# Kernel optimization log

Measured on AMD Instinct MI355X. Metric: run time of the kernel, lower is better.

Reference implementation:

```python
import jax, jax.numpy as jnp
import numpy as np

# static sizes
B = 32          # graphs
NPER = 1024     # nodes per graph
N0 = B * NPER
F_IN = 128
H = 4           # heads
DH = 32         # per-head dim (128/4)
HID = H * DH    # 128
E = 524288      # edges (avg degree 16)
K1, K2, K3 = 512, 256, 128  # ceil(0.5*nper) per stage
NC = 10


def gcn_agg(h, src, dst, w, n):
    """GCNConv propagation: sym-normalized aggregation with self-loops.
    h: [n,F] already projected; w: [E] edge weight (0 for filtered edges)."""
    deg = jax.ops.segment_sum(w, dst, num_segments=n) + 1.0  # +1 self-loop
    dinv = jax.lax.rsqrt(deg)
    coef = dinv[src] * dinv[dst] * w                          # [E]
    agg = jax.ops.segment_sum(h[src] * coef[:, None], dst, num_segments=n)
    return agg + h / deg[:, None]  # self-loop term: dinv[i]^2 = 1/deg[i]


def mh_gcn(x, W, b, src, dst, w, n):
    """MAGPoolGCNLayer: per-head GCNConv (32->32), relu, concat heads."""
    h = jnp.einsum('nhd,hde->nhe', x.reshape(n, H, DH), W).reshape(n, HID)
    return jax.nn.relu(gcn_agg(h, src, dst, w, n) + b.reshape(HID))


def att_pool(x, src, dst, w, A, psW, psb, n, k):
    """MultiHeadAtt: standard att, complex score, concat pooling, global weight."""
    sub = x.reshape(n, H, DH)
    att = jnp.einsum('nhd,hd->nh', sub, A)            # per-head Linear(32,1)
    cat = (att[:, :, None] * sub).reshape(n, HID)     # score*sub, concat
    score = (gcn_agg(cat @ psW, src, dst, w, n) + psb)[:, 0]  # GCNConv(HID,1)
    nper = n // B
    _, idx = jax.lax.top_k(score.reshape(B, nper), k)  # per-graph topk
    perm = (idx + jnp.arange(B)[:, None] * nper).reshape(-1)
    xn = x[perm] * jnp.tanh(score[perm])[:, None]      # global att weighting
    # filter_adj: remap kept nodes, mask edges touching dropped nodes
    nmap = jnp.full((n,), -1, jnp.int32).at[perm].set(jnp.arange(B * k, dtype=jnp.int32))
    ns, nd = nmap[src], nmap[dst]
    wn = w * ((ns >= 0) & (nd >= 0)).astype(w.dtype)
    return xn, jnp.maximum(ns, 0), jnp.maximum(nd, 0), wn


def readout(x):
    # graphs are contiguous with equal node counts -> reshape readout
    xr = x.reshape(B, -1, x.shape[-1])
    return jnp.concatenate([xr.max(1), xr.mean(1)], axis=1)  # [B, 2*HID]


def setup_inputs():
    key = jax.random.key(0)
    ks = jax.random.split(key, 26)
    gid = jnp.repeat(jnp.arange(B, dtype=jnp.int32), E // B)
    src = jax.random.randint(ks[0], (E,), 0, NPER, dtype=jnp.int32) + gid * NPER
    dst = jax.random.randint(ks[1], (E,), 0, NPER, dtype=jnp.int32) + gid * NPER
    x = jax.random.normal(ks[2], (N0, F_IN), jnp.float32)
    s = 0.1
    def rn(k, shp):
        return jax.random.normal(k, shp, jnp.float32) * s
    return {
        'x': x, 'src': src, 'dst': dst,
        'W1': rn(ks[3], (H, DH, DH)), 'b1': rn(ks[4], (H, DH)), 'A1': rn(ks[5], (H, DH)),
        'ps1W': rn(ks[6], (HID, 1)), 'ps1b': rn(ks[7], (1,)),
        'W2': rn(ks[8], (H, DH, DH)), 'b2': rn(ks[9], (H, DH)), 'A2': rn(ks[10], (H, DH)),
        'ps2W': rn(ks[11], (HID, 1)), 'ps2b': rn(ks[12], (1,)),
        'W3': rn(ks[13], (H, DH, DH)), 'b3': rn(ks[14], (H, DH)), 'A3': rn(ks[15], (H, DH)),
        'ps3W': rn(ks[16], (HID, 1)), 'ps3b': rn(ks[17], (1,)),
        'l1W': rn(ks[18], (2 * HID, HID)), 'l1b': rn(ks[19], (HID,)),
        'l2W': rn(ks[20], (HID, HID // 2)), 'l2b': rn(ks[21], (HID // 2,)),
        'l3W': rn(ks[22], (HID // 2, NC)), 'l3b': rn(ks[23], (NC,)),
    }


def reference(x, src, dst, W1, b1, A1, ps1W, ps1b, W2, b2, A2, ps2W, ps2b,
              W3, b3, A3, ps3W, ps3b, l1W, l1b, l2W, l2b, l3W, l3b):
    w = jnp.ones((E,), x.dtype)
    h = mh_gcn(x, W1, b1, src, dst, w, N0)
    h, s1, d1, w1 = att_pool(h, src, dst, w, A1, ps1W, ps1b, N0, K1)
    r1 = readout(h)
    n1 = B * K1
    h = mh_gcn(h, W2, b2, s1, d1, w1, n1)
    h, s2, d2, w2 = att_pool(h, s1, d1, w1, A2, ps2W, ps2b, n1, K2)
    r2 = readout(h)
    n2 = B * K2
    h = mh_gcn(h, W3, b3, s2, d2, w2, n2)
    h, _, _, _ = att_pool(h, s2, d2, w2, A3, ps3W, ps3b, n2, K3)
    r3 = readout(h)
    z = r1 + r2 + r3                      # [B, 2*HID]
    z = jax.nn.relu(z @ l1W + l1b)        # dropout skipped (eval mode)
    z = jax.nn.relu(z @ l2W + l2b)
    return jax.nn.log_softmax(z @ l3W + l3b, axis=-1)
```

## Files before the change

### kernel.cpp

```cpp
#include <hip/hip_runtime.h>
#include <math.h>

#define BGR 32
#define NPER0 1024
#define N0 (BGR * NPER0)
#define FDIM 128
#define EDG 524288
#define K1 512
#define K2 256
#define K3 128
#define EBLK (EDG / 256)
#define SXP 36
#define CAP 64

__device__ __forceinline__ unsigned enc_f(float v) {
    unsigned u = __float_as_uint(v);
    return (u & 0x80000000u) ? ~u : (u | 0x80000000u);
}
__device__ __forceinline__ float dec_f(unsigned u) {
    return (u & 0x80000000u) ? __uint_as_float(u ^ 0x80000000u) : __uint_as_float(~u);
}

__global__ void zero_all(int* __restrict__ cntA, unsigned* __restrict__ rmax,
                         float* __restrict__ rsum) {
    int i = blockIdx.x * 256 + threadIdx.x;
    if (i < N0) cntA[i] = 0;
    if (i < 3 * BGR * FDIM) { rmax[i] = 0u; rsum[i] = 0.0f; }
}

__device__ __forceinline__ void proj_compute(float* __restrict__ hp, int nb, int t,
                                             const float* __restrict__ sW,
                                             const float* __restrict__ sxT) {
    const int fg = t >> 3, ng = t & 7, h = fg >> 3;
    const float* ap = sxT + h * 32 * SXP + ng * 4;
    const float* bp = sW + h * 1024 + (fg & 7) * 4;
    float4 acc0 = {0.f, 0.f, 0.f, 0.f}, acc1 = acc0, acc2 = acc0, acc3 = acc0;
#pragma unroll
    for (int k = 0; k < 32; k++) {
        float4 a = *(const float4*)(ap + k * SXP);
        float4 b = *(const float4*)(bp + k * 32);
        acc0.x = fmaf(a.x, b.x, acc0.x); acc0.y = fmaf(a.x, b.y, acc0.y);
        acc0.z = fmaf(a.x, b.z, acc0.z); acc0.w = fmaf(a.x, b.w, acc0.w);
        acc1.x = fmaf(a.y, b.x, acc1.x); acc1.y = fmaf(a.y, b.y, acc1.y);
        acc1.z = fmaf(a.y, b.z, acc1.z); acc1.w = fmaf(a.y, b.w, acc1.w);
        acc2.x = fmaf(a.z, b.x, acc2.x); acc2.y = fmaf(a.z, b.y, acc2.y);
        acc2.z = fmaf(a.z, b.z, acc2.z); acc2.w = fmaf(a.z, b.w, acc2.w);
        acc3.x = fmaf(a.w, b.x, acc3.x); acc3.y = fmaf(a.w, b.y, acc3.y);
        acc3.z = fmaf(a.w, b.z, acc3.z); acc3.w = fmaf(a.w, b.w, acc3.w);
    }
    float4* op = (float4*)(hp + (size_t)(nb + ng * 4) * FDIM + fg * 4);
    op[0] = acc0; op[32] = acc1; op[64] = acc2; op[96] = acc3;
}

__device__ __forceinline__ void pool_body(const float* __restrict__ ha,
                                          const int* __restrict__ perm,
                                          const float* __restrict__ mult, int k, int pb,
                                          unsigned* __restrict__ rmax,
                                          float* __restrict__ rsum,
                                          float* __restrict__ smax,
                                          float* __restrict__ ssum) {
    const int t = threadIdx.x;
    const int g = pb & 31;
    const int c = pb >> 5;
    const int f = t & 127, half = t >> 7;
    const int base = g * k + c * 8;
    float vmax = -1e30f, vsum = 0.0f;
#pragma unroll
    for (int j0 = 0; j0 < 4; j0++) {
        int newid = base + half + j0 * 2;
        int old = perm[newid];
        float m = mult[newid];
        float v = ha[(size_t)old * FDIM + f] * m;
        vmax = fmaxf(vmax, v);
        vsum += v;
    }
    if (half) { smax[f] = vmax; ssum[f] = vsum; }
    __syncthreads();
    if (!half) {
        vmax = fmaxf(vmax, smax[f]);
        vsum += ssum[f];
        atomicMax(&rmax[g * FDIM + f], enc_f(vmax));
        atomicAdd(&rsum[g * FDIM + f], vsum);
    }
}

__global__ void bin_proj1(const int* __restrict__ src, const int* __restrict__ dst,
                          int* __restrict__ cnt, int* __restrict__ slot,
                          const float* __restrict__ x, const float* __restrict__ W,
                          float* __restrict__ hp) {
    __shared__ __align__(16) float sW[4096];
    __shared__ __align__(16) float sxT[128 * SXP];
    const int t = threadIdx.x;
    if (blockIdx.x < EBLK) {
        int e = blockIdx.x * 256 + t;
        int s = src[e];
        int d = dst[e];
        int p = atomicAdd(&cnt[d], 1);
        if (p < CAP) slot[d * CAP + p] = s;
        return;
    }
    const int tb = blockIdx.x - EBLK;
    const int nb = (tb & 31) * NPER0 + (tb >> 5) * 32;
    for (int i = t; i < 4096; i += 256) sW[i] = W[i];
    for (int i = t; i < 4096; i += 256) {
        int node = i >> 7, dim = i & 127;
        sxT[dim * SXP + node] = x[(size_t)(nb + node) * FDIM + dim];
    }
    __syncthreads();
    proj_compute(hp, nb, t, sW, sxT);
}

__global__ void bin_proj_pool(const int* __restrict__ cnt_prev,
                              const int* __restrict__ slot_prev,
                              const int* __restrict__ nmap,
                              int* __restrict__ cnt_next, int* __restrict__ slot_next,
                              const float* __restrict__ ha, const int* __restrict__ perm,
                              const float* __restrict__ mult, const float* __restrict__ W,
                              float* __restrict__ hp, int ncomp, int ntiles, int kprev,
                              unsigned* __restrict__ rmax, float* __restrict__ rsum) {
    __shared__ __align__(16) float sW[4096];
    __shared__ __align__(16) float sxT[128 * SXP];
    const int t = threadIdx.x;
    if (blockIdx.x < ncomp) {
        const int w = t >> 6, lane = t & 63;
        const int b = (blockIdx.x & 31) * kprev + (blockIdx.x >> 5) * 4 + w;
        const int old = perm[b];
        const int c = min(cnt_prev[old], CAP);
        int a = -1;
        if (lane < c) a = nmap[slot_prev[(size_t)old * CAP + lane]];
        unsigned long long mk = __ballot(a >= 0);
        if (a >= 0) {
            int pos = __popcll(mk & ((1ull << lane) - 1ull));
            slot_next[(size_t)b * CAP + pos] = a;
        }
        if (lane == 0) cnt_next[b] = __popcll(mk);
        return;
    }
    if (blockIdx.x >= ncomp + ntiles) {
        pool_body(ha, perm, mult, kprev, blockIdx.x - (ncomp + ntiles), rmax, rsum,
                  sW, sW + 128);
        return;
    }
    const int tb = blockIdx.x - ncomp;
    const int nb = (tb & 31) * kprev + (tb >> 5) * 32;
    for (int i = t; i < 4096; i += 256) sW[i] = W[i];
    for (int i = t; i < 4096; i += 256) {
        int node = i >> 7, dim = i & 127;
        int newid = nb + node;
        sxT[dim * SXP + node] = ha[(size_t)perm[newid] * FDIM + dim] * mult[newid];
    }
    __syncthreads();
    proj_compute(hp, nb, t, sW, sxT);
}

__global__ void pool_kernel(const float* __restrict__ ha, const int* __restrict__ perm,
                            const float* __restrict__ mult, int k,
                            unsigned* __restrict__ rmax, float* __restrict__ rsum) {
    __shared__ float smax[128], ssum[128];
    pool_body(ha, perm, mult, k, blockIdx.x, rmax, rsum, smax, ssum);
}

__global__ void agg_kernel(const float* __restrict__ hp, const float* __restrict__ b,
                           const int* __restrict__ cnt, const int* __restrict__ slot,
                           const float* __restrict__ A, const float* __restrict__ psW,
                           float* __restrict__ ha, float* __restrict__ csd, int nper) {
    const int w = threadIdx.x >> 6;
    const int lane = threadIdx.x & 63;
    const int g = blockIdx.x & 31;
    const int chunk = blockIdx.x >> 5;
    const int i = g * nper + chunk * 4 + w;
    const int ci = cnt[i];
    const float di = rsqrtf((float)ci + 1.0f);
    const int c = min(ci, CAP);
    const float2* __restrict__ hp2 = (const float2*)hp;
    float2 self = hp2[(size_t)i * 64 + lane];
    float accx = self.x * di * di, accy = self.y * di * di;
    int idx = 0;
    float dv = 0.0f;
    if (lane < c) {
        idx = slot[i * CAP + lane];
        dv = rsqrtf((float)cnt[idx] + 1.0f);
    }
    int j = 0;
    for (; j + 3 < c; j += 4) {
        int s0 = __shfl(idx, j, 64);
        int s1 = __shfl(idx, j + 1, 64);
        int s2 = __shfl(idx, j + 2, 64);
        int s3 = __shfl(idx, j + 3, 64);
        float c0 = __shfl(dv, j, 64) * di;
        float c1 = __shfl(dv, j + 1, 64) * di;
        float c2 = __shfl(dv, j + 2, 64) * di;
        float c3 = __shfl(dv, j + 3, 64) * di;
        float2 v0 = hp2[(size_t)s0 * 64 + lane];
        float2 v1 = hp2[(size_t)s1 * 64 + lane];
        float2 v2 = hp2[(size_t)s2 * 64 + lane];
        float2 v3 = hp2[(size_t)s3 * 64 + lane];
        accx = fmaf(v0.x, c0, accx); accy = fmaf(v0.y, c0, accy);
        accx = fmaf(v1.x, c1, accx); accy = fmaf(v1.y, c1, accy);
        accx = fmaf(v2.x, c2, accx); accy = fmaf(v2.y, c2, accy);
        accx = fmaf(v3.x, c3, accx); accy = fmaf(v3.y, c3, accy);
    }
    for (; j < c; j++) {
        int s = __shfl(idx, j, 64);
        float co = __shfl(dv, j, 64) * di;
        float2 v = hp2[(size_t)s * 64 + lane];
        accx = fmaf(v.x, co, accx); accy = fmaf(v.y, co, accy);
    }
    float2 bb = ((const float2*)b)[lane];
    float2 o;
    o.x = fmaxf(accx + bb.x, 0.0f);
    o.y = fmaxf(accy + bb.y, 0.0f);
    ((float2*)ha)[(size_t)i * 64 + lane] = o;
    float2 Av = ((const float2*)A)[lane];
    float2 Pv = ((const float2*)psW)[lane];
    float a = o.x * Av.x + o.y * Av.y;
    float p = o.x * Pv.x + o.y * Pv.y;
#pragma unroll
    for (int d = 8; d > 0; d >>= 1) {
        a += __shfl_down(a, d, 16);
        p += __shfl_down(p, d, 16);
    }
    float part = a * p;
    part += __shfl_down(part, 16, 64);
    part += __shfl_down(part, 32, 64);
    if (lane == 0) csd[i] = part * di;
}

__global__ void score_kernel(const float* __restrict__ csd, const int* __restrict__ cnt,
                             const int* __restrict__ slot, const float* __restrict__ psb,
                             float* __restrict__ scout, int nper) {
    const int w = threadIdx.x >> 6;
    const int lane = threadIdx.x & 63;
    const int g = blockIdx.x & 31;
    const int chunk = blockIdx.x >> 5;
    const int i = g * nper + chunk * 4 + w;
    const int ci = cnt[i];
    const int c = min(ci, CAP);
    float v = 0.0f;
    if (lane < c) v = csd[slot[(size_t)i * CAP + lane]];
#pragma unroll
    for (int d = 32; d > 0; d >>= 1) v += __shfl_xor(v, d, 64);
    if (lane == 0)
        scout[i] = rsqrtf((float)ci + 1.0f) * (v + csd[i]) + psb[0];
}

__global__ void topk_kernel(const float* __restrict__ scin, int nper, int k,
                            int* __restrict__ nmap, int* __restrict__ perm,
                            float* __restrict__ mult) {
    __shared__ float sc[NPER0];
    __shared__ unsigned ukey[NPER0];
    __shared__ unsigned hist[256];
    __shared__ unsigned wtot[4];
    __shared__ unsigned sel[2];
    __shared__ int ctr[2];
    const int g = blockIdx.x, t = threadIdx.x;
    const int w = t >> 6, l = t & 63;
    const int gnb = g * nper;
    for (int i = t; i < nper; i += 256) {
        float v = scin[gnb + i];
        sc[i] = v;
        ukey[i] = enc_f(v);
    }
    if (t == 0) { sel[0] = 0u; sel[1] = (unsigned)k; }
    __syncthreads();
    for (int shift = 24; shift >= 0; shift -= 8) {
        hist[t] = 0u;
        __syncthreads();
        const unsigned prefix = sel[0];
        const unsigned need = sel[1];
        for (int i = t; i < nper; i += 256) {
            unsigned u = ukey[i];
            bool inp = (shift == 24) || ((u >> (shift + 8)) == (prefix >> (shift + 8)));
            int dig = inp ? (int)((u >> shift) & 255u) : -1;
            int cv = inp ? 1 : 0;
#pragma unroll
            for (int d = 1; d < 64; d <<= 1) {
                int od = __shfl_xor(dig, d, 64);
                int oc = __shfl_xor(cv, d, 64);
                if (od == dig) cv = ((l & d) == 0) ? (cv + oc) : 0;
            }
            if (dig >= 0 && cv > 0) atomicAdd(&hist[dig], (unsigned)cv);
        }
        __syncthreads();
        const unsigned h = hist[t];
        unsigned s = h;
#pragma unroll
        for (int off = 1; off < 64; off <<= 1) {
            unsigned v = __shfl_down(s, off, 64);
            if (l + off < 64) s += v;
        }
        if (l == 0) wtot[w] = s;
        __syncthreads();
        unsigned add = 0;
        for (int ww = w + 1; ww < 4; ww++) add += wtot[ww];
        const unsigned sfx = s + add;
        const unsigned gtr = sfx - h;
        if (sfx >= need && gtr < need) {
            sel[0] = prefix | ((unsigned)t << shift);
            sel[1] = need - gtr;
        }
        __syncthreads();
    }
    const unsigned T = sel[0];
    const int need = (int)sel[1];
    if (t == 0) { ctr[0] = 0; ctr[1] = k - need; }
    __syncthreads();
    for (int i = t; i < nper; i += 256) {
        unsigned u = ukey[i];
        int node = gnb + i;
        int newid = -1;
        if (u > T) {
            newid = g * k + atomicAdd(&ctr[0], 1);
        } else if (u == T) {
            int slot2 = atomicAdd(&ctr[1], 1);
            if (slot2 < k) newid = g * k + slot2;
        }
        nmap[node] = newid;
        if (newid >= 0) {
            perm[newid] = node;
            mult[newid] = tanhf(sc[i]);
        }
    }
}

__global__ void final_mlp(const unsigned* __restrict__ rmax, const float* __restrict__ rsum,
                          const float* __restrict__ l1W, const float* __restrict__ l1b,
                          const float* __restrict__ l2W, const float* __restrict__ l2b,
                          const float* __restrict__ l3W, const float* __restrict__ l3b,
                          float* __restrict__ out) {
    __shared__ float sz[256], s1[128], s2[64], s3[10], red[2];
    const int g = blockIdx.x, t = threadIdx.x;
    const int RS = BGR * FDIM;
    sz[t] = dec_f(rmax[g * FDIM + t]) + dec_f(rmax[RS + g * FDIM + t]) +
            dec_f(rmax[2 * RS + g * FDIM + t]);
    sz[t + 128] = rsum[g * FDIM + t] / (float)K1 + rsum[RS + g * FDIM + t] / (float)K2 +
                  rsum[2 * RS + g * FDIM + t] / (float)K3;
    __syncthreads();
    float acc = l1b[t];
    for (int i = 0; i < 256; i++) acc = fmaf(sz[i], l1W[i * 128 + t], acc);
    s1[t] = fmaxf(acc, 0.0f);
    __syncthreads();
    if (t < 64) {
        float a2 = l2b[t];
        for (int i = 0; i < 128; i++) a2 = fmaf(s1[i], l2W[i * 64 + t], a2);
        s2[t] = fmaxf(a2, 0.0f);
    }
    __syncthreads();
    if (t < 10) {
        float a3 = l3b[t];
        for (int i = 0; i < 64; i++) a3 = fmaf(s2[i], l3W[i * 10 + t], a3);
        s3[t] = a3;
    }
    __syncthreads();
    if (t == 0) {
        float m = -1e30f;
        for (int c = 0; c < 10; c++) m = fmaxf(m, s3[c]);
        float sum = 0.0f;
        for (int c = 0; c < 10; c++) sum += expf(s3[c] - m);
        red[0] = m;
        red[1] = logf(sum);
    }
    __syncthreads();
    if (t < 10) out[g * 10 + t] = s3[t] - red[0] - red[1];
}

extern "C" void kernel_launch(void* const* d_in, const int* in_sizes, int n_in,
                              void* d_out, int out_size, void* d_ws, size_t ws_size,
                              hipStream_t stream) {
    const float* x    = (const float*)d_in[0];
    const int* src0   = (const int*)d_in[1];
    const int* dst0   = (const int*)d_in[2];
    const float* W1   = (const float*)d_in[3];
    const float* b1   = (const float*)d_in[4];
    const float* A1   = (const float*)d_in[5];
    const float* ps1W = (const float*)d_in[6];
    const float* ps1b = (const float*)d_in[7];
    const float* W2   = (const float*)d_in[8];
    const float* b2   = (const float*)d_in[9];
    const float* A2   = (const float*)d_in[10];
    const float* ps2W = (const float*)d_in[11];
    const float* ps2b = (const float*)d_in[12];
    const float* W3   = (const float*)d_in[13];
    const float* b3   = (const float*)d_in[14];
    const float* A3   = (const float*)d_in[15];
    const float* ps3W = (const float*)d_in[16];
    const float* ps3b = (const float*)d_in[17];
    const float* l1W  = (const float*)d_in[18];
    const float* l1b  = (const float*)d_in[19];
    const float* l2W  = (const float*)d_in[20];
    const float* l2b  = (const float*)d_in[21];
    const float* l3W  = (const float*)d_in[22];
    const float* l3b  = (const float*)d_in[23];
    float* out = (float*)d_out;

    char* ws = (char*)d_ws;
    size_t o = 0;
    auto alloc = [&](size_t bytes) -> void* {
        void* p = ws + o;
        o += (bytes + 255) & ~(size_t)255;
        return p;
    };
    float*    hproj = (float*)alloc((size_t)N0 * FDIM * 4);
    float*    hact  = (float*)alloc((size_t)N0 * FDIM * 4);
    int*      cntA  = (int*)alloc(N0 * 4);
    int*      cntB  = (int*)alloc(BGR * K1 * 4);
    int*      cntC  = (int*)alloc(BGR * K2 * 4);
    int*      slotA = (int*)alloc((size_t)N0 * CAP * 4);
    int*      slotB = (int*)alloc((size_t)BGR * K1 * CAP * 4);
    int*      slotC = (int*)alloc((size_t)BGR * K2 * CAP * 4);
    float*    cs    = (float*)alloc(N0 * 4);
    float*    scb   = (float*)alloc(N0 * 4);
    int*      nmapA = (int*)alloc(N0 * 4);
    int*      nmapB = (int*)alloc(BGR * K1 * 4);
    int*      nmapC = (int*)alloc(BGR * K2 * 4);
    int*      perm  = (int*)alloc(BGR * K1 * 4);
    float*    mult  = (float*)alloc(BGR * K1 * 4);
    unsigned* rmax  = (unsigned*)alloc(3 * BGR * FDIM * 4);
    float*    rsum  = (float*)alloc(3 * BGR * FDIM * 4);

    const int n1 = BGR * K1, n2 = BGR * K2;
    const int RS = BGR * FDIM;

    zero_all<<<N0 / 256, 256, 0, stream>>>(cntA, rmax, rsum);
    bin_proj1<<<EBLK + N0 / 32, 256, 0, stream>>>(src0, dst0, cntA, slotA, x, W1, hproj);
    agg_kernel<<<N0 / 4, 256, 0, stream>>>(hproj, b1, cntA, slotA, A1, ps1W, hact, cs, NPER0);
    score_kernel<<<N0 / 4, 256, 0, stream>>>(cs, cntA, slotA, ps1b, scb, NPER0);
    topk_kernel<<<BGR, 256, 0, stream>>>(scb, NPER0, K1, nmapA, perm, mult);

    bin_proj_pool<<<n1 / 4 + n1 / 32 + BGR * K1 / 8, 256, 0, stream>>>(
        cntA, slotA, nmapA, cntB, slotB, hact, perm, mult, W2, hproj,
        n1 / 4, n1 / 32, K1, rmax, rsum);
    agg_kernel<<<n1 / 4, 256, 0, stream>>>(hproj, b2, cntB, slotB, A2, ps2W, hact, cs, K1);
    score_kernel<<<n1 / 4, 256, 0, stream>>>(cs, cntB, slotB, ps2b, scb, K1);
    topk_kernel<<<BGR, 256, 0, stream>>>(scb, K1, K2, nmapB, perm, mult);

    bin_proj_pool<<<n2 / 4 + n2 / 32 + BGR * K2 / 8, 256, 0, stream>>>(
        cntB, slotB, nmapB, cntC, slotC, hact, perm, mult, W3, hproj,
        n2 / 4, n2 / 32, K2, rmax + RS, rsum + RS);
    agg_kernel<<<n2 / 4, 256, 0, stream>>>(hproj, b3, cntC, slotC, A3, ps3W, hact, cs, K2);
    score_kernel<<<n2 / 4, 256, 0, stream>>>(cs, cntC, slotC, ps3b, scb, K2);
    topk_kernel<<<BGR, 256, 0, stream>>>(scb, K2, K3, nmapC, perm, mult);

    pool_kernel<<<BGR * K3 / 8, 256, 0, stream>>>(hact, perm, mult, K3,
                                                  rmax + 2 * RS, rsum + 2 * RS);
    final_mlp<<<BGR, 128, 0, stream>>>(rmax, rsum, l1W, l1b, l2W, l2b, l3W, l3b, out);

    (void)in_sizes; (void)n_in; (void)out_size; (void)ws_size;
}
```

Before: 253.3 us.

## Fuse final pool into MLP kernel, coarsen pool blocks, reorder edge binning

The last-stage readout pool is folded into final_mlp, which now runs 256 threads per graph and reduces the kept nodes directly. This drops one launch and the third rmax/rsum atomic buffer. Pool blocks in bin_proj_pool now cover 32 nodes instead of 8, so there are fewer blocks and fewer atomics. Edge binning blocks are interleaved across graphs, which may spread atomic contention on cnt. The cost is less parallelism in the fused final kernel, where each of 32 blocks reads 128 rows serially.

```diff
diff --git a/kernel.cpp b/kernel.cpp
--- a/kernel.cpp
+++ b/kernel.cpp
@@ -10,6 +10,7 @@
 #define K2 256
 #define K3 128
 #define EBLK (EDG / 256)
+#define EPG (EDG / BGR)
 #define SXP 36
 #define CAP 64
 
@@ -25,7 +26,7 @@
                          float* __restrict__ rsum) {
     int i = blockIdx.x * 256 + threadIdx.x;
     if (i < N0) cntA[i] = 0;
-    if (i < 3 * BGR * FDIM) { rmax[i] = 0u; rsum[i] = 0.0f; }
+    if (i < 2 * BGR * FDIM) { rmax[i] = 0u; rsum[i] = 0.0f; }
 }
 
 __device__ __forceinline__ void proj_compute(float* __restrict__ hp, int nb, int t,
@@ -63,10 +64,10 @@
     const int g = pb & 31;
     const int c = pb >> 5;
     const int f = t & 127, half = t >> 7;
-    const int base = g * k + c * 8;
+    const int base = g * k + c * 32;
     float vmax = -1e30f, vsum = 0.0f;
 #pragma unroll
-    for (int j0 = 0; j0 < 4; j0++) {
+    for (int j0 = 0; j0 < 16; j0++) {
         int newid = base + half + j0 * 2;
         int old = perm[newid];
         float m = mult[newid];
@@ -92,7 +93,8 @@
     __shared__ __align__(16) float sxT[128 * SXP];
     const int t = threadIdx.x;
     if (blockIdx.x < EBLK) {
-        int e = blockIdx.x * 256 + t;
+        const int g = blockIdx.x & 31, chunk = blockIdx.x >> 5;
+        int e = g * EPG + chunk * 256 + t;
         int s = src[e];
         int d = dst[e];
         int p = atomicAdd(&cnt[d], 1);
@@ -153,13 +155,6 @@
     proj_compute(hp, nb, t, sW, sxT);
 }
 
-__global__ void pool_kernel(const float* __restrict__ ha, const int* __restrict__ perm,
-                            const float* __restrict__ mult, int k,
-                            unsigned* __restrict__ rmax, float* __restrict__ rsum) {
-    __shared__ float smax[128], ssum[128];
-    pool_body(ha, perm, mult, k, blockIdx.x, rmax, rsum, smax, ssum);
-}
-
 __global__ void agg_kernel(const float* __restrict__ hp, const float* __restrict__ b,
                            const int* __restrict__ cnt, const int* __restrict__ slot,
                            const float* __restrict__ A, const float* __restrict__ psW,
@@ -323,22 +318,42 @@
     }
 }
 
-__global__ void final_mlp(const unsigned* __restrict__ rmax, const float* __restrict__ rsum,
+__global__ void final_mlp(const float* __restrict__ ha, const int* __restrict__ perm,
+                          const float* __restrict__ mult,
+                          const unsigned* __restrict__ rmax, const float* __restrict__ rsum,
                           const float* __restrict__ l1W, const float* __restrict__ l1b,
                           const float* __restrict__ l2W, const float* __restrict__ l2b,
                           const float* __restrict__ l3W, const float* __restrict__ l3b,
                           float* __restrict__ out) {
-    __shared__ float sz[256], s1[128], s2[64], s3[10], red[2];
+    __shared__ float sz[256], s1[128], s2[64], s3[10], red[2], sm2[128], ss2[128];
     const int g = blockIdx.x, t = threadIdx.x;
     const int RS = BGR * FDIM;
-    sz[t] = dec_f(rmax[g * FDIM + t]) + dec_f(rmax[RS + g * FDIM + t]) +
-            dec_f(rmax[2 * RS + g * FDIM + t]);
-    sz[t + 128] = rsum[g * FDIM + t] / (float)K1 + rsum[RS + g * FDIM + t] / (float)K2 +
-                  rsum[2 * RS + g * FDIM + t] / (float)K3;
-    __syncthreads();
-    float acc = l1b[t];
-    for (int i = 0; i < 256; i++) acc = fmaf(sz[i], l1W[i * 128 + t], acc);
-    s1[t] = fmaxf(acc, 0.0f);
+    const int f = t & 127, half = t >> 7;
+    float vmax = -1e30f, vsum = 0.0f;
+#pragma unroll 8
+    for (int j0 = 0; j0 < 64; j0++) {
+        int newid = g * K3 + half + j0 * 2;
+        int old = perm[newid];
+        float m = mult[newid];
+        float v = ha[(size_t)old * FDIM + f] * m;
+        vmax = fmaxf(vmax, v);
+        vsum += v;
+    }
+    if (half) { sm2[f] = vmax; ss2[f] = vsum; }
+    __syncthreads();
+    if (!half) {
+        vmax = fmaxf(vmax, sm2[f]);
+        vsum += ss2[f];
+        sz[f] = dec_f(rmax[g * FDIM + f]) + dec_f(rmax[RS + g * FDIM + f]) + vmax;
+        sz[f + 128] = rsum[g * FDIM + f] / (float)K1 + rsum[RS + g * FDIM + f] / (float)K2 +
+                      vsum / (float)K3;
+    }
+    __syncthreads();
+    if (t < 128) {
+        float acc = l1b[t];
+        for (int i = 0; i < 256; i++) acc = fmaf(sz[i], l1W[i * 128 + t], acc);
+        s1[t] = fmaxf(acc, 0.0f);
+    }
     __syncthreads();
     if (t < 64) {
         float a2 = l2b[t];
@@ -415,8 +430,8 @@
     int*      nmapC = (int*)alloc(BGR * K2 * 4);
     int*      perm  = (int*)alloc(BGR * K1 * 4);
     float*    mult  = (float*)alloc(BGR * K1 * 4);
-    unsigned* rmax  = (unsigned*)alloc(3 * BGR * FDIM * 4);
-    float*    rsum  = (float*)alloc(3 * BGR * FDIM * 4);
+    unsigned* rmax  = (unsigned*)alloc(2 * BGR * FDIM * 4);
+    float*    rsum  = (float*)alloc(2 * BGR * FDIM * 4);
 
     const int n1 = BGR * K1, n2 = BGR * K2;
     const int RS = BGR * FDIM;
@@ -427,23 +442,22 @@
     score_kernel<<<N0 / 4, 256, 0, stream>>>(cs, cntA, slotA, ps1b, scb, NPER0);
     topk_kernel<<<BGR, 256, 0, stream>>>(scb, NPER0, K1, nmapA, perm, mult);
 
-    bin_proj_pool<<<n1 / 4 + n1 / 32 + BGR * K1 / 8, 256, 0, stream>>>(
+    bin_proj_pool<<<n1 / 4 + n1 / 32 + BGR * K1 / 32, 256, 0, stream>>>(
         cntA, slotA, nmapA, cntB, slotB, hact, perm, mult, W2, hproj,
         n1 / 4, n1 / 32, K1, rmax, rsum);
     agg_kernel<<<n1 / 4, 256, 0, stream>>>(hproj, b2, cntB, slotB, A2, ps2W, hact, cs, K1);
     score_kernel<<<n1 / 4, 256, 0, stream>>>(cs, cntB, slotB, ps2b, scb, K1);
     topk_kernel<<<BGR, 256, 0, stream>>>(scb, K1, K2, nmapB, perm, mult);
 
-    bin_proj_pool<<<n2 / 4 + n2 / 32 + BGR * K2 / 8, 256, 0, stream>>>(
+    bin_proj_pool<<<n2 / 4 + n2 / 32 + BGR * K2 / 32, 256, 0, stream>>>(
         cntB, slotB, nmapB, cntC, slotC, hact, perm, mult, W3, hproj,
         n2 / 4, n2 / 32, K2, rmax + RS, rsum + RS);
     agg_kernel<<<n2 / 4, 256, 0, stream>>>(hproj, b3, cntC, slotC, A3, ps3W, hact, cs, K2);
     score_kernel<<<n2 / 4, 256, 0, stream>>>(cs, cntC, slotC, ps3b, scb, K2);
     topk_kernel<<<BGR, 256, 0, stream>>>(scb, K2, K3, nmapC, perm, mult);
 
-    pool_kernel<<<BGR * K3 / 8, 256, 0, stream>>>(hact, perm, mult, K3,
-                                                  rmax + 2 * RS, rsum + 2 * RS);
-    final_mlp<<<BGR, 128, 0, stream>>>(rmax, rsum, l1W, l1b, l2W, l2b, l3W, l3b, out);
+    final_mlp<<<BGR, 256, 0, stream>>>(hact, perm, mult, rmax, rsum,
+                                       l1W, l1b, l2W, l2b, l3W, l3b, out);
 
     (void)in_sizes; (void)n_in; (void)out_size; (void)ws_size;
 }
```

After: 260.2 us. +2.7%, slower.
